# Performance work log

Measured on AMD Instinct MI355X. Metric: run time of the kernel, lower is better.

The kernel has to match this reference:

```python
import jax, jax.numpy as jnp
import numpy as np

S, H = 8192, 7168          # tokens, hidden
D0, D1 = 1536, 576         # q_a_proj dim, kv_a_proj_with_mqa dim (output_offset = [0, 1536, 2112])
R = 64                     # LoRA rank per slice


def setup_inputs() -> dict:
    key = jax.random.key(0)
    k1, k2, k3, k4, k5 = jax.random.split(key, 5)
    x = jax.random.normal(k1, (S, H), dtype=jnp.float32)
    W = jax.random.normal(k2, (D0 + D1, H), dtype=jnp.float32) * 0.02
    bias = jax.random.normal(k3, (D0 + D1,), dtype=jnp.float32) * 0.02
    # stacked LoRA-A for both slices: [n_slices*r, hidden]
    A_buffer = jax.random.normal(k4, (2 * R, H), dtype=jnp.float32) * 0.02
    # LoRA-B padded to max slice dim: [n_slices, max_out_dim, r]; only first D1 rows of slice 1 are valid
    B_buffer = jax.random.normal(k5, (2, D0, R), dtype=jnp.float32) * 0.02
    return {"x": x, "W": W, "bias": bias, "A_buffer": A_buffer, "B_buffer": B_buffer}


def reference(x, W, bias, A_buffer, B_buffer):
    # base replicated linear: [S, D0+D1]
    out = jnp.einsum('sh,oh->so', x, W) + bias
    # fused LoRA-A for both slices: [S, 2*R]
    la = jnp.einsum('sh,rh->sr', x, A_buffer)
    # segmented LoRA-B (run_qkv_lora with n_slices=2): scatter-add into offset slices
    out = out.at[:, :D0].add(jnp.einsum('sr,or->so', la[:, :R], B_buffer[0, :D0]))
    out = out.at[:, D0:].add(jnp.einsum('sr,or->so', la[:, R:], B_buffer[1, :D1]))
    return out
```

## Files before the change

kernel.cpp:

```cpp
#include <hip/hip_runtime.h>
#include <hip/hip_bf16.h>

#define S_DIM 8192
#define H_DIM 7168
#define D0_DIM 1536
#define D1_DIM 576
#define N_DIM 2112
#define R_DIM 64
#define LA_WIDTH 128

#define K_EXT 7296
#define NT32 228
#define N_PAD 2176
#define KSPLIT 8
#define KCHUNK 896

#define XE_RB 512
#define WE_RB 136

#define CONV_BLKS 256
#define CONV_ITEMS (WE_RB * NT32 * 64)

typedef __attribute__((ext_vector_type(4))) float f32x4;
typedef __attribute__((ext_vector_type(8))) short bf16x8;
typedef __attribute__((ext_vector_type(4))) short bf16x4;

__device__ __forceinline__ short f2bf(float f) {
    union { __hip_bfloat16 h; short s; } u;
    u.h = __float2bfloat16(f);
    return u.s;
}

__device__ __forceinline__ bf16x8 pack8(f32x4 a, f32x4 b) {
    bf16x8 r;
    r[0] = f2bf(a[0]); r[1] = f2bf(a[1]); r[2] = f2bf(a[2]); r[3] = f2bf(a[3]);
    r[4] = f2bf(b[0]); r[5] = f2bf(b[1]); r[6] = f2bf(b[2]); r[7] = f2bf(b[3]);
    return r;
}

__device__ __forceinline__ void gload_lds16(const short* g, short* l) {
    __builtin_amdgcn_global_load_lds(
        (const __attribute__((address_space(1))) unsigned int*)(const void*)g,
        (__attribute__((address_space(3))) unsigned int*)(void*)l, 16, 0, 0);
}

__global__ __launch_bounds__(256, 2)
void fused_stage1(const float* __restrict__ x, const float* __restrict__ W,
                  const float* __restrict__ A, const float* __restrict__ Bbuf,
                  float* __restrict__ la, short* __restrict__ xe,
                  short* __restrict__ we) {
    if (blockIdx.x < CONV_BLKS) {
        const unsigned base0 = blockIdx.x * 256u + threadIdx.x;
#pragma unroll 1
        for (int itr = 0; itr < 31; ++itr) {
            unsigned id = base0 + (unsigned)itr * (CONV_BLKS * 256u);
            if (id < CONV_ITEMS) {
                unsigned rb  = id / 14592u;
                unsigned rem = id % 14592u;
                unsigned kb  = rem >> 6, sl = rem & 63u;
                unsigned r16 = sl >> 2;
                unsigned c   = (sl & 3u) ^ (((r16 >> 3) & 1u) << 1);
                unsigned row = rb * 16u + r16;
                bf16x8 v = {};
                if (row < N_DIM) {
                    if (kb < 224u) {
                        unsigned k = kb * 32u + c * 8u;
                        const float* p = W + (size_t)row * H_DIM + k;
                        f32x4 a = *(const f32x4*)p;
                        f32x4 b = *(const f32x4*)(p + 4);
                        v = pack8(a, b);
                    } else {
                        unsigned kl = (kb - 224u) * 32u + c * 8u;
                        const bool s1 = row >= D0_DIM;
                        const unsigned lo = s1 ? 64u : 0u;
                        if (kl >= lo && kl < lo + 64u) {
                            const float* p = Bbuf + ((size_t)(s1 ? 1u : 0u) * D0_DIM +
                                                     (row - (s1 ? D0_DIM : 0u))) * R_DIM + (kl - lo);
                            f32x4 a = *(const f32x4*)p;
                            f32x4 b = *(const f32x4*)(p + 4);
                            v = pack8(a, b);
                        }
                    }
                }
                *(bf16x8*)(we + ((size_t)rb * NT32 + kb) * 512u + sl * 8u) = v;
            }
        }
        return;
    }

    __shared__ __align__(16) short sX[2][128 * 40];
    __shared__ __align__(16) short sA[2][128 * 40];

    const int bx = blockIdx.x - CONV_BLKS;
    const int tid = threadIdx.x;
    const int m0 = (bx >> 3) * 128;
    const int k0 = (bx & 7) * KCHUNK;
    const int wave = tid >> 6, lane = tid & 63;
    const int wm = (wave & 1) * 64, wn = (wave >> 1) * 64;
    const int fr = lane & 15, fq = lane >> 4;

    f32x4 acc[4][4] = {};

    const int srow = tid >> 1, shalf = (tid & 1) * 16;
    const float* xP = x + (size_t)(m0 + srow) * H_DIM + k0 + shalf;
    const float* aP = A + (size_t)srow * H_DIM + k0 + shalf;

    const unsigned rbx = (unsigned)(m0 + srow) >> 4;
    const unsigned r16 = (unsigned)srow & 15u;
    const unsigned kb0 = (unsigned)k0 >> 5;
    const unsigned c0  = (unsigned)shalf >> 3;
    const unsigned sx  = ((r16 >> 3) & 1u) << 1;
    const unsigned sl0 = r16 * 4u + (c0 ^ sx);
    const unsigned sl1 = r16 * 4u + ((c0 + 1u) ^ sx);
    short* xeB = xe + ((size_t)rbx * NT32 + kb0) * 512u;

    const int swoff = srow * 40 + shalf;
    const int xr_off = (wm + fr) * 40 + fq * 8;
    const int ar_off = (wn + fr) * 40 + fq * 8;

    f32x4 cx0 = *(const f32x4*)(xP);
    f32x4 cx1 = *(const f32x4*)(xP + 4);
    f32x4 cx2 = *(const f32x4*)(xP + 8);
    f32x4 cx3 = *(const f32x4*)(xP + 12);
    f32x4 ca0 = *(const f32x4*)(aP);
    f32x4 ca1 = *(const f32x4*)(aP + 4);
    f32x4 ca2 = *(const f32x4*)(aP + 8);
    f32x4 ca3 = *(const f32x4*)(aP + 12);
    f32x4 nx0 = {}, nx1 = {}, nx2 = {}, nx3 = {};
    f32x4 na0 = {}, na1 = {}, na2 = {}, na3 = {};

#pragma unroll 1
    for (int it = 0; it < KCHUNK / 32; ++it) {
        if (it < KCHUNK / 32 - 1) {
            const float* px = xP + (it + 1) * 32;
            const float* pa = aP + (it + 1) * 32;
            nx0 = *(const f32x4*)(px);
            nx1 = *(const f32x4*)(px + 4);
            nx2 = *(const f32x4*)(px + 8);
            nx3 = *(const f32x4*)(px + 12);
            na0 = *(const f32x4*)(pa);
            na1 = *(const f32x4*)(pa + 4);
            na2 = *(const f32x4*)(pa + 8);
            na3 = *(const f32x4*)(pa + 12);
        }
        bf16x8 px0 = pack8(cx0, cx1), px1 = pack8(cx2, cx3);
        bf16x8 pa0 = pack8(ca0, ca1), pa1 = pack8(ca2, ca3);

        *(bf16x8*)(xeB + (size_t)it * 512 + sl0 * 8u) = px0;
        *(bf16x8*)(xeB + (size_t)it * 512 + sl1 * 8u) = px1;

        short* bX = &sX[it & 1][0];
        short* bA = &sA[it & 1][0];
        *(bf16x8*)(bX + swoff) = px0; *(bf16x8*)(bX + swoff + 8) = px1;
        *(bf16x8*)(bA + swoff) = pa0; *(bf16x8*)(bA + swoff + 8) = pa1;

        asm volatile("s_waitcnt lgkmcnt(0)" ::: "memory");
        __builtin_amdgcn_s_barrier();
        __builtin_amdgcn_sched_barrier(0);

        bf16x8 af[4], bfg[4];
#pragma unroll
        for (int i = 0; i < 4; ++i) af[i] = *(const bf16x8*)(bX + xr_off + i * 640);
#pragma unroll
        for (int i = 0; i < 4; ++i) bfg[i] = *(const bf16x8*)(bA + ar_off + i * 640);
#pragma unroll
        for (int mi = 0; mi < 4; ++mi)
#pragma unroll
            for (int ni = 0; ni < 4; ++ni)
                acc[mi][ni] = __builtin_amdgcn_mfma_f32_16x16x32_bf16(
                    af[mi], bfg[ni], acc[mi][ni], 0, 0, 0);

        cx0 = nx0; cx1 = nx1; cx2 = nx2; cx3 = nx3;
        ca0 = na0; ca1 = na1; ca2 = na2; ca3 = na3;
    }

#pragma unroll
    for (int ni = 0; ni < 4; ++ni) {
        const int col = wn + ni * 16 + fr;
#pragma unroll
        for (int mi = 0; mi < 4; ++mi) {
            const int row = m0 + wm + mi * 16 + fq * 4;
#pragma unroll
            for (int r = 0; r < 4; ++r)
                atomicAdd(&la[(size_t)(row + r) * LA_WIDTH + col], acc[mi][ni][r]);
        }
    }
}

__global__ __launch_bounds__(256)
void la_to_xe(const float* __restrict__ la, short* __restrict__ xe) {
    unsigned id = blockIdx.x * 256u + threadIdx.x;
    unsigned row = id >> 4, c8 = (id & 15u) * 8u;
    const float* p = la + (size_t)row * LA_WIDTH + c8;
    f32x4 s0 = *(const f32x4*)(p);
    f32x4 s1 = *(const f32x4*)(p + 4);
    unsigned rbx = row >> 4, r16 = row & 15u;
    unsigned kb = 224u + (c8 >> 5);
    unsigned cc = (c8 >> 3) & 3u;
    unsigned sl = r16 * 4u + (cc ^ (((r16 >> 3) & 1u) << 1));
    *(bf16x8*)(xe + ((size_t)rbx * NT32 + kb) * 512u + sl * 8u) = pack8(s0, s1);
}

__global__ __launch_bounds__(256, 2)
void main_gemm_tiled(const short* __restrict__ xe, const short* __restrict__ we,
                     const float* __restrict__ bias, float* __restrict__ out) {
    __shared__ __align__(16) short lds[2 * 12288];

    const int tid = threadIdx.x;
    const int bx = blockIdx.x;
    const int xcd = bx & 7, p = bx >> 3;
    const int tile = xcd * 68 + p;
    const int m0 = (tile / 17) * 256;
    const int n0 = (tile % 17) * 128;

    const int wave = tid >> 6, lane = tid & 63;
    const int wm = (wave & 1) * 128;
    const int wn = (wave >> 1) * 64;
    const int fr = lane & 15, fq = lane >> 4;

    f32x4 acc[8][4] = {};

    const short* gp[6];
    int ldoff[6];
    {
        const short* xe_pan = xe + (size_t)(m0 >> 4) * NT32 * 512 + lane * 8;
        const short* we_pan = we + (size_t)(n0 >> 4) * NT32 * 512 + lane * 8;
#pragma unroll
        for (int i = 0; i < 6; ++i) {
            const int idx = wave * 6 + i;
            if (idx < 16) { gp[i] = xe_pan + (size_t)idx * NT32 * 512; ldoff[i] = idx * 512; }
            else          { gp[i] = we_pan + (size_t)(idx - 16) * NT32 * 512; ldoff[i] = 8192 + (idx - 16) * 512; }
        }
    }

    const int swz  = (fq ^ ((fr >> 3) << 1)) * 8;
    const int aoff = (wm + fr) * 32 + swz;
    const int boff = 8192 + (wn + fr) * 32 + swz;

#pragma unroll
    for (int i = 0; i < 6; ++i) gload_lds16(gp[i], lds + ldoff[i]);
#pragma unroll
    for (int i = 0; i < 6; ++i) gload_lds16(gp[i] + 512, lds + 12288 + ldoff[i]);

#pragma unroll 1
    for (int kt = 0; kt < NT32; ++kt) {
        const int b = kt & 1;
        asm volatile("s_waitcnt vmcnt(6)" ::: "memory");
        __builtin_amdgcn_s_barrier();
        __builtin_amdgcn_sched_barrier(0);

        const short* pa = lds + b * 12288 + aoff;
        const short* pb = lds + b * 12288 + boff;
        bf16x8 af[8], brf[4];
#pragma unroll
        for (int m = 0; m < 8; ++m) af[m] = *(const bf16x8*)(pa + m * 512);
#pragma unroll
        for (int n = 0; n < 4; ++n) brf[n] = *(const bf16x8*)(pb + n * 512);

        asm volatile("s_waitcnt lgkmcnt(0)" ::: "memory");
        __builtin_amdgcn_sched_barrier(0);
        __builtin_amdgcn_s_barrier();

        int tt = kt + 2; if (tt >= NT32) tt -= NT32;
#pragma unroll
        for (int i = 0; i < 6; ++i)
            gload_lds16(gp[i] + (size_t)tt * 512, lds + b * 12288 + ldoff[i]);
        __builtin_amdgcn_sched_barrier(0);

        __builtin_amdgcn_s_setprio(1);
#pragma unroll
        for (int m = 0; m < 8; ++m)
#pragma unroll
            for (int n = 0; n < 4; ++n)
                acc[m][n] = __builtin_amdgcn_mfma_f32_16x16x32_bf16(
                    af[m], brf[n], acc[m][n], 0, 0, 0);
        __builtin_amdgcn_s_setprio(0);
        __builtin_amdgcn_sched_barrier(0);
    }
    asm volatile("s_waitcnt vmcnt(0)" ::: "memory");

#pragma unroll
    for (int n = 0; n < 4; ++n) {
        const int col = n0 + wn + n * 16 + fr;
        if (col < N_DIM) {
            const float bv = bias[col];
#pragma unroll
            for (int m = 0; m < 8; ++m) {
                const int row = m0 + wm + m * 16 + fq * 4;
#pragma unroll
                for (int r = 0; r < 4; ++r)
                    out[(size_t)(row + r) * N_DIM + col] = acc[m][n][r] + bv;
            }
        }
    }
}

__global__ __launch_bounds__(256, 2)
void lora_a_gemm(const float* __restrict__ x, const float* __restrict__ Abuf,
                 float* __restrict__ la) {
    __shared__ __align__(16) short sX[32 * 40];
    __shared__ __align__(16) short sA[128 * 40];
    const int tid = threadIdx.x;
    const int m0 = blockIdx.x * 32;
    const int wave = tid >> 6, lane = tid & 63;
    const int fr = lane & 15, fq = lane >> 4;
    const int wn = wave * 32;
    f32x4 acc[2][2] = {};
    const int xrow = tid >> 3, xcol = (tid & 7) * 4;
    const float* xP = x + (size_t)(m0 + xrow) * H_DIM + xcol;
    short* sXw = sX + xrow * 40 + xcol;
    const int arow = tid >> 1, ahalf = (tid & 1) * 16;
    const float* aP = Abuf + (size_t)arow * H_DIM + ahalf;
    short* sAw = sA + arow * 40 + ahalf;
    const short* sXr = sX + fr * 40 + fq * 8;
    const short* sAr = sA + (wn + fr) * 40 + fq * 8;
    for (int kt = 0; kt < H_DIM / 32; ++kt) {
        f32x4 xv = *(const f32x4*)(xP + kt * 32);
        f32x4 a0 = *(const f32x4*)(aP + kt * 32);
        f32x4 a1 = *(const f32x4*)(aP + kt * 32 + 4);
        f32x4 a2 = *(const f32x4*)(aP + kt * 32 + 8);
        f32x4 a3 = *(const f32x4*)(aP + kt * 32 + 12);
        bf16x4 xs;
        xs[0] = f2bf(xv[0]); xs[1] = f2bf(xv[1]);
        xs[2] = f2bf(xv[2]); xs[3] = f2bf(xv[3]);
        bf16x8 as0 = pack8(a0, a1), as1 = pack8(a2, a3);
        __syncthreads();
        *(bf16x4*)(sXw) = xs;
        *(bf16x8*)(sAw) = as0;
        *(bf16x8*)(sAw + 8) = as1;
        __syncthreads();
        bf16x8 xf0 = *(const bf16x8*)(sXr);
        bf16x8 xf1 = *(const bf16x8*)(sXr + 16 * 40);
        bf16x8 af0 = *(const bf16x8*)(sAr);
        bf16x8 af1 = *(const bf16x8*)(sAr + 16 * 40);
        acc[0][0] = __builtin_amdgcn_mfma_f32_16x16x32_bf16(xf0, af0, acc[0][0], 0, 0, 0);
        acc[0][1] = __builtin_amdgcn_mfma_f32_16x16x32_bf16(xf0, af1, acc[0][1], 0, 0, 0);
        acc[1][0] = __builtin_amdgcn_mfma_f32_16x16x32_bf16(xf1, af0, acc[1][0], 0, 0, 0);
        acc[1][1] = __builtin_amdgcn_mfma_f32_16x16x32_bf16(xf1, af1, acc[1][1], 0, 0, 0);
    }
#pragma unroll
    for (int ni = 0; ni < 2; ++ni) {
        const int col = wn + ni * 16 + fr;
#pragma unroll
        for (int mi = 0; mi < 2; ++mi) {
            const int row = m0 + mi * 16 + fq * 4;
#pragma unroll
            for (int r = 0; r < 4; ++r)
                la[(size_t)(row + r) * LA_WIDTH + col] = acc[mi][ni][r];
        }
    }
}

#define LDS_STRIDE 40
__global__ __launch_bounds__(256, 2)
void main_gemm(const float* __restrict__ x, const float* __restrict__ W,
               const float* __restrict__ bias, const float* __restrict__ Bbuf,
               const float* __restrict__ la, float* __restrict__ out) {
    __shared__ __align__(16) short sA[128 * LDS_STRIDE];
    __shared__ __align__(16) short sB[128 * LDS_STRIDE];
    const int tid = threadIdx.x;
    const int n0 = blockIdx.x * 128, m0 = blockIdx.y * 128;
    const int wave = tid >> 6, lane = tid & 63;
    const int wm = (wave & 1) * 64, wn = (wave >> 1) * 64;
    const int fr = lane & 15, fq = lane >> 4;
    f32x4 acc[4][4] = {};
    const int srow = tid >> 1, shalf = (tid & 1) * 16;
    const float* xP = x + (size_t)(m0 + srow) * H_DIM + shalf;
    const int wRow = n0 + srow;
    const bool wValid = wRow < N_DIM;
    const float* wP = W + (size_t)wRow * H_DIM + shalf;
    const int slice = (n0 >= D0_DIM) ? 1 : 0;
    const int oCol = wRow - slice * D0_DIM;
    const bool bValid = wValid && (oCol < (slice ? D1_DIM : D0_DIM));
    const float* laP = la + (size_t)(m0 + srow) * LA_WIDTH + slice * R_DIM + shalf;
    const float* bP = Bbuf + ((size_t)slice * D0_DIM + oCol) * R_DIM + shalf;
    short* sAw = sA + srow * LDS_STRIDE + shalf;
    short* sBw = sB + srow * LDS_STRIDE + shalf;
    const short* sAr = sA + (wm + fr) * LDS_STRIDE + fq * 8;
    const short* sBr = sB + (wn + fr) * LDS_STRIDE + fq * 8;
    const int KT = H_DIM / 32;
    for (int it = 0; it < KT + 2; ++it) {
        const float *pa, *pb;
        bool vb;
        if (it < KT) { pa = xP + it * 32; pb = wP + it * 32; vb = wValid; }
        else { const int lt = it - KT; pa = laP + lt * 32; pb = bP + lt * 32; vb = bValid; }
        f32x4 a0 = *(const f32x4*)(pa);
        f32x4 a1 = *(const f32x4*)(pa + 4);
        f32x4 a2 = *(const f32x4*)(pa + 8);
        f32x4 a3 = *(const f32x4*)(pa + 12);
        f32x4 z = {0.f, 0.f, 0.f, 0.f};
        f32x4 b0 = z, b1 = z, b2 = z, b3 = z;
        if (vb) {
            b0 = *(const f32x4*)(pb); b1 = *(const f32x4*)(pb + 4);
            b2 = *(const f32x4*)(pb + 8); b3 = *(const f32x4*)(pb + 12);
        }
        bf16x8 pa0 = pack8(a0, a1), pa1 = pack8(a2, a3);
        bf16x8 pb0 = pack8(b0, b1), pb1 = pack8(b2, b3);
        __syncthreads();
        *(bf16x8*)(sAw) = pa0; *(bf16x8*)(sAw + 8) = pa1;
        *(bf16x8*)(sBw) = pb0; *(bf16x8*)(sBw + 8) = pb1;
        __syncthreads();
        bf16x8 af[4], bfg[4];
#pragma unroll
        for (int i = 0; i < 4; ++i) af[i] = *(const bf16x8*)(sAr + i * 16 * LDS_STRIDE);
#pragma unroll
        for (int i = 0; i < 4; ++i) bfg[i] = *(const bf16x8*)(sBr + i * 16 * LDS_STRIDE);
#pragma unroll
        for (int mi = 0; mi < 4; ++mi)
#pragma unroll
            for (int ni = 0; ni < 4; ++ni)
                acc[mi][ni] = __builtin_amdgcn_mfma_f32_16x16x32_bf16(
                    af[mi], bfg[ni], acc[mi][ni], 0, 0, 0);
    }
#pragma unroll
    for (int ni = 0; ni < 4; ++ni) {
        const int col = n0 + wn + ni * 16 + fr;
        if (col < N_DIM) {
            const float bv = bias[col];
#pragma unroll
            for (int mi = 0; mi < 4; ++mi) {
                const int row = m0 + wm + mi * 16 + fq * 4;
#pragma unroll
                for (int r = 0; r < 4; ++r)
                    out[(size_t)(row + r) * N_DIM + col] = acc[mi][ni][r] + bv;
            }
        }
    }
}

extern "C" void kernel_launch(void* const* d_in, const int* in_sizes, int n_in,
                              void* d_out, int out_size, void* d_ws, size_t ws_size,
                              hipStream_t stream) {
    const float* x    = (const float*)d_in[0];
    const float* W    = (const float*)d_in[1];
    const float* bias = (const float*)d_in[2];
    const float* A    = (const float*)d_in[3];
    const float* B    = (const float*)d_in[4];
    float* out = (float*)d_out;

    const size_t xe_bytes = (size_t)XE_RB * NT32 * 1024;
    const size_t we_bytes = (size_t)WE_RB * NT32 * 1024;
    const size_t la_bytes = (size_t)S_DIM * LA_WIDTH * 4;

    if (ws_size >= xe_bytes + we_bytes) {
        short* xe = (short*)d_ws;
        short* we = (short*)((char*)d_ws + xe_bytes);
        float* la = (float*)d_out;

        hipMemsetAsync(d_out, 0, la_bytes, stream);
        fused_stage1<<<dim3(CONV_BLKS + 512), dim3(256), 0, stream>>>(
            x, W, A, B, la, xe, we);
        la_to_xe<<<dim3(S_DIM * 16 / 256), dim3(256), 0, stream>>>(la, xe);
        main_gemm_tiled<<<dim3(32 * 17), dim3(256), 0, stream>>>(xe, we, bias, out);
    } else {
        float* la = (float*)d_ws;
        lora_a_gemm<<<dim3(S_DIM / 32), dim3(256), 0, stream>>>(x, A, la);
        main_gemm<<<dim3(N_DIM / 128 + 1, S_DIM / 128), dim3(256), 0, stream>>>(
            x, W, bias, B, la, out);
    }
}
```

Baseline: 703.9 us.

## Triple-buffer LDS and interleave LDS reads, prefetch, and MFMA in GEMM loop

Moves the main GEMM from a double-buffered LDS scheme to three rotating LDS buffers. With the extra buffer, the loop drops the second barrier and the full lgkmcnt wait, and issues global-to-LDS prefetches into a buffer that is not being read. LDS fragment reads, global loads and MFMA groups are interleaved in four phases so that memory work overlaps with matrix math. LDS use per block grows by half, which could reduce occupancy at two blocks per CU. Correctness now depends on the compiler inserting the right lgkmcnt waits between the LDS reads and the MFMAs that use them.

```diff
diff --git a/kernel.cpp b/kernel.cpp
--- a/kernel.cpp
+++ b/kernel.cpp
@@ -201,10 +201,16 @@
     *(bf16x8*)(xe + ((size_t)rbx * NT32 + kb) * 512u + sl * 8u) = pack8(s0, s1);
 }
 
+#define MFMA_ROW(m, a)                                                          \
+    acc[m][0] = __builtin_amdgcn_mfma_f32_16x16x32_bf16(a, brf0, acc[m][0], 0, 0, 0); \
+    acc[m][1] = __builtin_amdgcn_mfma_f32_16x16x32_bf16(a, brf1, acc[m][1], 0, 0, 0); \
+    acc[m][2] = __builtin_amdgcn_mfma_f32_16x16x32_bf16(a, brf2, acc[m][2], 0, 0, 0); \
+    acc[m][3] = __builtin_amdgcn_mfma_f32_16x16x32_bf16(a, brf3, acc[m][3], 0, 0, 0)
+
 __global__ __launch_bounds__(256, 2)
 void main_gemm_tiled(const short* __restrict__ xe, const short* __restrict__ we,
                      const float* __restrict__ bias, float* __restrict__ out) {
-    __shared__ __align__(16) short lds[2 * 12288];
+    __shared__ __align__(16) short lds[3 * 12288];
 
     const int tid = threadIdx.x;
     const int bx = blockIdx.x;
@@ -242,40 +248,68 @@
 #pragma unroll
     for (int i = 0; i < 6; ++i) gload_lds16(gp[i] + 512, lds + 12288 + ldoff[i]);
 
+    int bufo = 0;
+    int dbufo = 2 * 12288;
+    int toff = 2 * 512;
+
 #pragma unroll 1
     for (int kt = 0; kt < NT32; ++kt) {
-        const int b = kt & 1;
+        const short* pa = lds + bufo + aoff;
+        const short* pb = lds + bufo + boff;
+        short* st = lds + dbufo;
+        const int go = toff;
+
         asm volatile("s_waitcnt vmcnt(6)" ::: "memory");
         __builtin_amdgcn_s_barrier();
         __builtin_amdgcn_sched_barrier(0);
 
-        const short* pa = lds + b * 12288 + aoff;
-        const short* pb = lds + b * 12288 + boff;
-        bf16x8 af[8], brf[4];
-#pragma unroll
-        for (int m = 0; m < 8; ++m) af[m] = *(const bf16x8*)(pa + m * 512);
-#pragma unroll
-        for (int n = 0; n < 4; ++n) brf[n] = *(const bf16x8*)(pb + n * 512);
-
-        asm volatile("s_waitcnt lgkmcnt(0)" ::: "memory");
-        __builtin_amdgcn_sched_barrier(0);
-        __builtin_amdgcn_s_barrier();
-
-        int tt = kt + 2; if (tt >= NT32) tt -= NT32;
-#pragma unroll
-        for (int i = 0; i < 6; ++i)
-            gload_lds16(gp[i] + (size_t)tt * 512, lds + b * 12288 + ldoff[i]);
-        __builtin_amdgcn_sched_barrier(0);
-
+        bf16x8 brf0 = *(const bf16x8*)(pb);
+        bf16x8 brf1 = *(const bf16x8*)(pb + 512);
+        bf16x8 brf2 = *(const bf16x8*)(pb + 1024);
+        bf16x8 brf3 = *(const bf16x8*)(pb + 1536);
+        bf16x8 af0  = *(const bf16x8*)(pa);
+        bf16x8 af1  = *(const bf16x8*)(pa + 512);
+        gload_lds16(gp[0] + go, st + ldoff[0]);
+        gload_lds16(gp[1] + go, st + ldoff[1]);
+        __builtin_amdgcn_sched_barrier(0);
+
+        bf16x8 af2 = *(const bf16x8*)(pa + 1024);
+        bf16x8 af3 = *(const bf16x8*)(pa + 1536);
+        gload_lds16(gp[2] + go, st + ldoff[2]);
+        gload_lds16(gp[3] + go, st + ldoff[3]);
         __builtin_amdgcn_s_setprio(1);
-#pragma unroll
-        for (int m = 0; m < 8; ++m)
-#pragma unroll
-            for (int n = 0; n < 4; ++n)
-                acc[m][n] = __builtin_amdgcn_mfma_f32_16x16x32_bf16(
-                    af[m], brf[n], acc[m][n], 0, 0, 0);
+        MFMA_ROW(0, af0);
+        MFMA_ROW(1, af1);
         __builtin_amdgcn_s_setprio(0);
         __builtin_amdgcn_sched_barrier(0);
+
+        bf16x8 af4 = *(const bf16x8*)(pa + 2048);
+        bf16x8 af5 = *(const bf16x8*)(pa + 2560);
+        gload_lds16(gp[4] + go, st + ldoff[4]);
+        gload_lds16(gp[5] + go, st + ldoff[5]);
+        __builtin_amdgcn_s_setprio(1);
+        MFMA_ROW(2, af2);
+        MFMA_ROW(3, af3);
+        __builtin_amdgcn_s_setprio(0);
+        __builtin_amdgcn_sched_barrier(0);
+
+        bf16x8 af6 = *(const bf16x8*)(pa + 3072);
+        bf16x8 af7 = *(const bf16x8*)(pa + 3584);
+        __builtin_amdgcn_s_setprio(1);
+        MFMA_ROW(4, af4);
+        MFMA_ROW(5, af5);
+        __builtin_amdgcn_s_setprio(0);
+        __builtin_amdgcn_sched_barrier(0);
+
+        __builtin_amdgcn_s_setprio(1);
+        MFMA_ROW(6, af6);
+        MFMA_ROW(7, af7);
+        __builtin_amdgcn_s_setprio(0);
+        __builtin_amdgcn_sched_barrier(0);
+
+        bufo += 12288;  if (bufo == 3 * 12288) bufo = 0;
+        dbufo += 12288; if (dbufo == 3 * 12288) dbufo = 0;
+        toff += 512;    if (toff == NT32 * 512) toff = 0;
     }
     asm volatile("s_waitcnt vmcnt(0)" ::: "memory");
 
```

Result: no change. 690.8 us (-1.9%).
